# Optimization experiments

Hardware: AMD Instinct MI355X
Metric: run time of the kernel (lower is better)

The kernel has to match this reference:

```python
import jax, jax.numpy as jnp
import numpy as np

N_NODES = 50000
EPS = 1e-16


def seg_softmax(att, seg, n):
    # att: [E, H], softmax over edges sharing the same destination (seg)
    m = jax.ops.segment_max(att, seg, num_segments=n)
    m = jnp.where(jnp.isfinite(m), m, 0.0)
    e = jnp.exp(att - m[seg])
    s = jax.ops.segment_sum(e, seg, num_segments=n)
    return e / (s[seg] + EPS)


def gat_layer(x, W, b, a_l, a_r, row, col, n, nhead, out_feats, alpha, act):
    h = (x @ W).reshape(-1, nhead, out_feats)           # [N, H, F]
    h = jnp.nan_to_num(h)
    h_l = jnp.sum(a_l * h, axis=-1)                     # [N, H]
    h_r = jnp.sum(a_r * h, axis=-1)                     # [N, H]
    e = h_l[row] + h_r[col]                             # [E, H]
    e = jax.nn.leaky_relu(e, negative_slope=alpha)
    att = seg_softmax(e, row, n)                        # softmax per destination node
    # sparse multi-head aggregation: out[i] = sum_{e: row[e]=i} att[e] * h[col[e]]
    msg = att[:, :, None] * h[col]                      # [E, H, F]
    out = jax.ops.segment_sum(msg, row, num_segments=n) # [N, H, F]
    out = out.reshape(n, nhead * out_feats) + b
    if act:
        out = jax.nn.relu(out)
    return out


def setup_inputs() -> dict:
    key = jax.random.key(0)
    ks = jax.random.split(key, 10)
    N, E = N_NODES, 800000
    x = jax.random.normal(ks[0], (N, 256), dtype=jnp.float32)
    row = jax.random.randint(ks[1], (E,), 0, N)
    col = jax.random.randint(ks[2], (E,), 0, N)
    g = 1.414  # xavier-like scale handled via normal * small std
    W1 = jax.random.normal(ks[3], (256, 128), dtype=jnp.float32) * (g / np.sqrt(256 + 128))
    b1 = jnp.zeros((128,), dtype=jnp.float32)
    al1 = jax.random.normal(ks[4], (1, 4, 32), dtype=jnp.float32) * 0.1
    ar1 = jax.random.normal(ks[5], (1, 4, 32), dtype=jnp.float32) * 0.1
    W2 = jax.random.normal(ks[6], (128, 64), dtype=jnp.float32) * (g / np.sqrt(128 + 64))
    b2 = jnp.zeros((64,), dtype=jnp.float32)
    al2 = jax.random.normal(ks[7], (1, 1, 64), dtype=jnp.float32) * 0.1
    ar2 = jax.random.normal(ks[8], (1, 1, 64), dtype=jnp.float32) * 0.1
    return {"x": x, "row": row, "col": col, "W1": W1, "b1": b1, "al1": al1,
            "ar1": ar1, "W2": W2, "b2": b2, "al2": al2, "ar2": ar2}


def reference(x, row, col, W1, b1, al1, ar1, W2, b2, al2, ar2):
    n = N_NODES
    h = gat_layer(x, W1, b1, al1, ar1, row, col, n, nhead=4, out_feats=32, alpha=0.2, act=True)
    out = gat_layer(h, W2, b2, al2, ar2, row, col, n, nhead=1, out_feats=64, alpha=0.2, act=False)
    return out
```

## Files before the change

kernel.cpp:

```cpp
#include <hip/hip_runtime.h>
#include <hip/hip_bf16.h>
#include <hip/hip_fp16.h>
#include <math.h>

#define ALPHA 0.2f
#define LOG2E 1.44269504088896f
#define CAP 8192

typedef _Float16 half8 __attribute__((ext_vector_type(8)));
typedef float f32x4 __attribute__((ext_vector_type(4)));

__global__ __launch_bounds__(256) void setup_kernel(
    int* __restrict__ gcursor,
    const float* __restrict__ W1, _Float16* __restrict__ W1t,
    const float* __restrict__ W2, _Float16* __restrict__ W2t) {
    const int blk = blockIdx.x, tid = threadIdx.x;
    if (blk == 0) {
        gcursor[tid] = 0;
    } else if (blk <= 128) {
        int i = (blk - 1) * 256 + tid;
        int k = i >> 7, c = i & 127;
        W1t[c * 256 + k] = (_Float16)W1[i];
    } else {
        int j = (blk - 129) * 256 + tid;
        int k = j >> 6, c = j & 63;
        W2t[c * 128 + k] = (_Float16)W2[j];
    }
}


__device__ __forceinline__ void part_body(char* smem, int blk,
                                          const int* __restrict__ row,
                                          const int* __restrict__ col,
                                          int* __restrict__ gcursor,
                                          unsigned* __restrict__ tmp, int E) {
    int* h = (int*)smem;
    int* rsv = h + 256;
    const int tid = threadIdx.x;
    const int base = blk * 4096;
    h[tid] = 0;
    __syncthreads();
#pragma unroll
    for (int k = 0; k < 16; ++k) {
        int i = base + k * 256 + tid;
        if (i < E) atomicAdd(&h[row[i] >> 8], 1);
    }
    __syncthreads();
    if (h[tid]) rsv[tid] = atomicAdd(&gcursor[tid], h[tid]);
    __syncthreads();
    h[tid] = 0;
    __syncthreads();
#pragma unroll
    for (int k = 0; k < 16; ++k) {
        int i = base + k * 256 + tid;
        if (i < E) {
            int r = row[i];
            int b = r >> 8;
            int loc = atomicAdd(&h[b], 1);
            tmp[(size_t)b * CAP + rsv[b] + loc] = ((unsigned)r << 16) | (unsigned)col[i];
        }
    }
}

__device__ __forceinline__ void bucket_body(char* smem, int k,
                                            const unsigned* __restrict__ tmp,
                                            const int* __restrict__ gcursor,
                                            unsigned* __restrict__ startcnt,
                                            unsigned short* __restrict__ csr_col, int N) {
    int* h = (int*)smem;
    int* rs = h + 256;
    int* wtot = rs + 256;
    const int tid = threadIdx.x;
    const int lane = tid & 63, wid = tid >> 6;
    const int base = k * CAP;
    const int count = gcursor[k];
    h[tid] = 0;
    __syncthreads();
    for (int p = tid; p < count; p += 256) atomicAdd(&h[(tmp[base + p] >> 16) & 255], 1);
    __syncthreads();
    int v = h[tid];
    int sc = v;
#pragma unroll
    for (int d = 1; d < 64; d <<= 1) {
        int u = __shfl_up(sc, d);
        if (lane >= d) sc += u;
    }
    if (lane == 63) wtot[wid] = sc;
    __syncthreads();
    int add = 0;
    for (int w = 0; w < wid; ++w) add += wtot[w];
    rs[tid] = sc - v + add + base;
    __syncthreads();
    int gr = k * 256 + tid;
    if (gr < N) startcnt[gr] = ((unsigned)rs[tid] << 11) | (unsigned)v;
    h[tid] = 0;
    __syncthreads();
    for (int p = tid; p < count; p += 256) {
        unsigned t = tmp[base + p];
        int rl = (t >> 16) & 255;
        int loc = atomicAdd(&h[rl], 1);
        csr_col[rs[rl] + loc] = (unsigned short)(t & 0xFFFF);
    }
}

__device__ __forceinline__ void gemm1_body(char* smem, int tile,
                                           const float* __restrict__ x,
                                           const _Float16* __restrict__ Wt,
                                           const float* __restrict__ al,
                                           const float* __restrict__ ar,
                                           _Float16* __restrict__ h,
                                           float* __restrict__ hl,
                                           float* __restrict__ hr, int N) {
    _Float16* xs = (_Float16*)smem;
    const int tid = threadIdx.x;
    const int lane = tid & 63, wc = tid >> 6;
    const int row0 = tile * 32;
    const int col0 = wc * 32;

#pragma unroll
    for (int it = 0; it < 8; ++it) {
        int i = it * 256 + tid;
        int r = i >> 6, c4 = i & 63;
        int gr = row0 + r;
        float4 v = {0.f, 0.f, 0.f, 0.f};
        if (gr < N) v = *(const float4*)(x + (size_t)gr * 256 + c4 * 4);
        union { _Float16 p[4]; uint2 u; } pk;
        pk.p[0] = (_Float16)v.x; pk.p[1] = (_Float16)v.y;
        pk.p[2] = (_Float16)v.z; pk.p[3] = (_Float16)v.w;
        int byte = r * 512 + c4 * 8;
        byte ^= (r & 7) << 4;
        *reinterpret_cast<uint2*>(smem + byte) = pk.u;
    }

    const _Float16* wbase = Wt + (size_t)(col0 + (lane & 15)) * 256 + (lane >> 4) * 8;

    __syncthreads();

    f32x4 acc[2][2] = {};
    half8 bf0[2], bf1[2], af0[2], af1[2];

    auto loadB = [&](int s, half8* dst) {
        dst[0] = *(const half8*)(wbase + s * 32);
        dst[1] = *(const half8*)(wbase + 16 * 256 + s * 32);
    };
    auto loadA = [&](int s, half8* dst) {
#pragma unroll
        for (int m = 0; m < 2; ++m) {
            int r = m * 16 + (lane & 15);
            int byte = r * 512 + s * 64 + (lane >> 4) * 16;
            byte ^= (r & 7) << 4;
            dst[m] = *reinterpret_cast<const half8*>(smem + byte);
        }
    };
    auto domfma = [&](half8* a, half8* bvec) {
#pragma unroll
        for (int m = 0; m < 2; ++m)
#pragma unroll
            for (int n = 0; n < 2; ++n)
                acc[m][n] = __builtin_amdgcn_mfma_f32_16x16x32_f16(
                    a[m], bvec[n], acc[m][n], 0, 0, 0);
    };

    loadB(0, bf0); loadA(0, af0);
#pragma unroll
    for (int s = 0; s < 8; s += 2) {
        if (s + 1 < 8) { loadB(s + 1, bf1); loadA(s + 1, af1); }
        domfma(af0, bf0);
        if (s + 2 < 8) { loadB(s + 2, bf0); loadA(s + 2, af0); }
        if (s + 1 < 8) domfma(af1, bf1);
    }

#pragma unroll
    for (int m = 0; m < 2; ++m) {
        int grow_base = row0 + m * 16 + (lane >> 4) * 4;
#pragma unroll
        for (int n = 0; n < 2; ++n) {
            int gcol = col0 + n * 16 + (lane & 15);
#pragma unroll
            for (int reg = 0; reg < 4; ++reg) {
                int grow = grow_base + reg;
                if (grow < N) h[(size_t)grow * 128 + gcol] = (_Float16)acc[m][n][reg];
            }
        }
    }

    const float al0 = al[col0 + (lane & 15)],      ar0 = ar[col0 + (lane & 15)];
    const float al1 = al[col0 + 16 + (lane & 15)], ar1 = ar[col0 + 16 + (lane & 15)];
#pragma unroll
    for (int m = 0; m < 2; ++m) {
#pragma unroll
        for (int reg = 0; reg < 4; ++reg) {
            float l = al0 * acc[m][0][reg] + al1 * acc[m][1][reg];
            float r = ar0 * acc[m][0][reg] + ar1 * acc[m][1][reg];
#pragma unroll
            for (int msk = 1; msk < 16; msk <<= 1) {
                l += __shfl_xor(l, msk);
                r += __shfl_xor(r, msk);
            }
            int grow = row0 + m * 16 + (lane >> 4) * 4 + reg;
            if ((lane & 15) == 0 && grow < N) {
                hl[grow * 4 + wc] = l * LOG2E;
                hr[grow * 4 + wc] = r * LOG2E;
            }
        }
    }
}

__global__ __launch_bounds__(256) void ka_kernel(
    const int* __restrict__ row, const int* __restrict__ col,
    int* __restrict__ gcursor, unsigned* __restrict__ tmp, int E, int eblocks,
    const float* __restrict__ x, const _Float16* __restrict__ W1t,
    const float* __restrict__ al, const float* __restrict__ ar,
    _Float16* __restrict__ h, float* __restrict__ hl, float* __restrict__ hr,
    int N, int tile0)
{
    __shared__ __align__(16) char smem[16384];
    if (blockIdx.x < (unsigned)eblocks)
        part_body(smem, blockIdx.x, row, col, gcursor, tmp, E);
    else
        gemm1_body(smem, tile0 + blockIdx.x - eblocks, x, W1t, al, ar, h, hl, hr, N);
}

__global__ __launch_bounds__(256) void kb_kernel(
    const unsigned* __restrict__ tmp, const int* __restrict__ gcursor,
    unsigned* __restrict__ startcnt, unsigned short* __restrict__ csr_col,
    int nbuck,
    const float* __restrict__ x, const _Float16* __restrict__ W1t,
    const float* __restrict__ al, const float* __restrict__ ar,
    _Float16* __restrict__ h, float* __restrict__ hl, float* __restrict__ hr,
    int N, int tile0)
{
    __shared__ __align__(16) char smem[16384];
    if (blockIdx.x < (unsigned)nbuck)
        bucket_body(smem, blockIdx.x, tmp, gcursor, startcnt, csr_col, N);
    else
        gemm1_body(smem, tile0 + blockIdx.x - nbuck, x, W1t, al, ar, h, hl, hr, N);
}

__global__ __launch_bounds__(256) void gemm2_mfma(
    const _Float16* __restrict__ xin, const _Float16* __restrict__ Wt,
    const float* __restrict__ al, const float* __restrict__ ar,
    _Float16* __restrict__ h, float* __restrict__ hl, float* __restrict__ hr, int N)
{
    __shared__ _Float16 xs[32 * 128];
    __shared__ float plds[32][4], prds[32][4];
    const int tid = threadIdx.x;
    const int lane = tid & 63, wc = tid >> 6;
    const int row0 = blockIdx.x * 32;
    const int col0 = wc * 16;

#pragma unroll
    for (int it = 0; it < 2; ++it) {
        int i = it * 256 + tid;
        int r = i >> 4, c16 = i & 15;
        int gr = row0 + r;
        uint4 v = {0, 0, 0, 0};
        if (gr < N) v = *(const uint4*)(xin + (size_t)gr * 128 + c16 * 8);
        int byte = r * 256 + c16 * 16;
        byte ^= (r & 7) << 4;
        *reinterpret_cast<uint4*>(reinterpret_cast<char*>(xs) + byte) = v;
    }

    const _Float16* wbase = Wt + (size_t)(col0 + (lane & 15)) * 128 + (lane >> 4) * 8;

    __syncthreads();

    f32x4 acc[2] = {};
    half8 bf0, bf1, af0[2], af1[2];

    auto loadA = [&](int s, half8* dst) {
#pragma unroll
        for (int m = 0; m < 2; ++m) {
            int r = m * 16 + (lane & 15);
            int byte = r * 256 + s * 64 + (lane >> 4) * 16;
            byte ^= (r & 7) << 4;
            dst[m] = *reinterpret_cast<const half8*>(
                reinterpret_cast<const char*>(xs) + byte);
        }
    };

    bf0 = *(const half8*)(wbase); loadA(0, af0);
#pragma unroll
    for (int s = 0; s < 4; s += 2) {
        if (s + 1 < 4) { bf1 = *(const half8*)(wbase + (s + 1) * 32); loadA(s + 1, af1); }
#pragma unroll
        for (int m = 0; m < 2; ++m)
            acc[m] = __builtin_amdgcn_mfma_f32_16x16x32_f16(af0[m], bf0, acc[m], 0, 0, 0);
        if (s + 2 < 4) { bf0 = *(const half8*)(wbase + (s + 2) * 32); loadA(s + 2, af0); }
        if (s + 1 < 4)
#pragma unroll
            for (int m = 0; m < 2; ++m)
                acc[m] = __builtin_amdgcn_mfma_f32_16x16x32_f16(af1[m], bf1, acc[m], 0, 0, 0);
    }

#pragma unroll
    for (int m = 0; m < 2; ++m) {
        int grow_base = row0 + m * 16 + (lane >> 4) * 4;
        int gcol = col0 + (lane & 15);
#pragma unroll
        for (int reg = 0; reg < 4; ++reg) {
            int grow = grow_base + reg;
            if (grow < N) h[(size_t)grow * 64 + gcol] = (_Float16)acc[m][reg];
        }
    }

    const float alv = al[col0 + (lane & 15)], arv = ar[col0 + (lane & 15)];
#pragma unroll
    for (int m = 0; m < 2; ++m) {
#pragma unroll
        for (int reg = 0; reg < 4; ++reg) {
            float l = alv * acc[m][reg];
            float r = arv * acc[m][reg];
#pragma unroll
            for (int msk = 1; msk < 16; msk <<= 1) {
                l += __shfl_xor(l, msk);
                r += __shfl_xor(r, msk);
            }
            int ri = m * 16 + (lane >> 4) * 4 + reg;
            if ((lane & 15) == 0) { plds[ri][wc] = l; prds[ri][wc] = r; }
        }
    }
    __syncthreads();
    if (tid < 32) {
        int grow = row0 + tid;
        if (grow < N) {
            float l = plds[tid][0] + plds[tid][1] + plds[tid][2] + plds[tid][3];
            float r = prds[tid][0] + prds[tid][1] + prds[tid][2] + prds[tid][3];
            hl[grow] = l * LOG2E;
            hr[grow] = r * LOG2E;
        }
    }
}

__global__ __launch_bounds__(256) void agg1_kernel(
    const unsigned* __restrict__ startcnt, const unsigned short* __restrict__ csr_col,
    const float* __restrict__ hls, const float* __restrict__ hrs,
    const _Float16* __restrict__ h, const float* __restrict__ b,
    _Float16* __restrict__ out, int N)
{
    const int i = blockIdx.x * 4 + (threadIdx.x >> 6);
    if (i >= N) return;
    const int lane = threadIdx.x & 63;
    const int q = lane >> 4;
    const int fl = lane & 15;
    const int head = fl >> 2;
    const unsigned pk = startcnt[i];
    const int s = (int)(pk >> 11), e = s + (int)(pk & 2047);
    const float hlv = hls[i * 4 + head];

    float acc[8] = {};
    float den = 0.f;

    int p0 = s + q;
    bool v0 = p0 < e;
    int cc0 = v0 ? (int)csr_col[p0] : 0;
    float hr0 = hrs[cc0 * 4 + head];
    uint4 g0 = *(const uint4*)(h + (size_t)cc0 * 128 + 8 * fl);

#pragma unroll 2
    for (int pb = s; pb < e; pb += 4) {
        int p1 = pb + 4 + q;
        bool v1 = p1 < e;
        int cc1 = v1 ? (int)csr_col[p1] : 0;
        float hr1v = hrs[cc1 * 4 + head];
        uint4 g1 = *(const uint4*)(h + (size_t)cc1 * 128 + 8 * fl);

        float sc = hlv + hr0;
        sc = sc > 0.f ? sc : ALPHA * sc;
        float w = exp2f(sc);
        w = v0 ? w : 0.f;
        den += w;
        union { uint4 u; _Float16 q8[8]; } hv; hv.u = g0;
#pragma unroll
        for (int k = 0; k < 8; ++k) acc[k] = fmaf(w, (float)hv.q8[k], acc[k]);

        v0 = v1; cc0 = cc1; hr0 = hr1v; g0 = g1;
    }

    den += __shfl_xor(den, 16); den += __shfl_xor(den, 32);
#pragma unroll
    for (int k = 0; k < 8; ++k) {
        acc[k] += __shfl_xor(acc[k], 16);
        acc[k] += __shfl_xor(acc[k], 32);
    }

    if (lane < 16) {
        float r = 1.f / (den + 1e-16f);
        const float* bp = b + 8 * fl;
        union { uint4 u; _Float16 q8[8]; } ov;
#pragma unroll
        for (int k = 0; k < 8; ++k) {
            float o = acc[k] * r + bp[k];
            o = o > 0.f ? o : 0.f;
            ov.q8[k] = (_Float16)o;
        }
        *reinterpret_cast<uint4*>(out + (size_t)i * 128 + 8 * fl) = ov.u;
    }
}

__global__ __launch_bounds__(256) void agg2_kernel(
    const unsigned* __restrict__ startcnt, const unsigned short* __restrict__ csr_col,
    const float* __restrict__ hls, const float* __restrict__ hrs,
    const _Float16* __restrict__ h, const float* __restrict__ b,
    float* __restrict__ out, int N)
{
    const int i = blockIdx.x * 4 + (threadIdx.x >> 6);
    if (i >= N) return;
    const int lane = threadIdx.x & 63;
    const int q = lane >> 4;
    const int fl = lane & 15;
    const unsigned pk = startcnt[i];
    const int s = (int)(pk >> 11), e = s + (int)(pk & 2047);
    const float hlv = hls[i];

    float acc[4] = {};
    float den = 0.f;

    int p0 = s + q;
    bool v0 = p0 < e;
    int cc0 = v0 ? (int)csr_col[p0] : 0;
    float hr0 = hrs[cc0];
    uint2 g0 = *(const uint2*)(h + (size_t)cc0 * 64 + 4 * fl);

#pragma unroll 2
    for (int pb = s; pb < e; pb += 4) {
        int p1 = pb + 4 + q;
        bool v1 = p1 < e;
        int cc1 = v1 ? (int)csr_col[p1] : 0;
        float hr1v = hrs[cc1];
        uint2 g1 = *(const uint2*)(h + (size_t)cc1 * 64 + 4 * fl);

        float sc = hlv + hr0;
        sc = sc > 0.f ? sc : ALPHA * sc;
        float w = exp2f(sc);
        w = v0 ? w : 0.f;
        den += w;
        union { uint2 u; _Float16 q4[4]; } hv; hv.u = g0;
#pragma unroll
        for (int k = 0; k < 4; ++k) acc[k] = fmaf(w, (float)hv.q4[k], acc[k]);

        v0 = v1; cc0 = cc1; hr0 = hr1v; g0 = g1;
    }

    den += __shfl_xor(den, 16); den += __shfl_xor(den, 32);
#pragma unroll
    for (int k = 0; k < 4; ++k) {
        acc[k] += __shfl_xor(acc[k], 16);
        acc[k] += __shfl_xor(acc[k], 32);
    }

    if (lane < 16) {
        float r = 1.f / (den + 1e-16f);
        float4 bv = *(const float4*)(b + 4 * fl);
        float4 ov;
        ov.x = acc[0] * r + bv.x;
        ov.y = acc[1] * r + bv.y;
        ov.z = acc[2] * r + bv.z;
        ov.w = acc[3] * r + bv.w;
        *reinterpret_cast<float4*>(out + (size_t)i * 64 + 4 * fl) = ov;
    }
}

extern "C" void kernel_launch(void* const* d_in, const int* in_sizes, int n_in,
                              void* d_out, int out_size, void* d_ws, size_t ws_size,
                              hipStream_t stream)
{
    const float* x   = (const float*)d_in[0];
    const int*   row = (const int*)d_in[1];
    const int*   col = (const int*)d_in[2];
    const float* W1  = (const float*)d_in[3];
    const float* b1  = (const float*)d_in[4];
    const float* al1 = (const float*)d_in[5];
    const float* ar1 = (const float*)d_in[6];
    const float* W2  = (const float*)d_in[7];
    const float* b2  = (const float*)d_in[8];
    const float* al2 = (const float*)d_in[9];
    const float* ar2 = (const float*)d_in[10];
    const int N = in_sizes[0] / 256;
    const int E = in_sizes[1];
    const int nbuck = (N + 255) >> 8;
    float* out = (float*)d_out;

    size_t off_b = 0;
    auto alloc = [&](size_t bytes) -> void* {
        void* p = (char*)d_ws + off_b;
        off_b += (bytes + 255) & ~(size_t)255;
        return p;
    };
    int*            gcursor  = (int*)alloc((size_t)256 * 4);
    unsigned*       startcnt = (unsigned*)alloc((size_t)N * 4);
    unsigned*       tmp      = (unsigned*)alloc((size_t)nbuck * CAP * 4);
    unsigned short* csr_col  = (unsigned short*)alloc((size_t)nbuck * CAP * 2 + 32);
    _Float16*       W1t      = (_Float16*)alloc((size_t)128 * 256 * 2);
    _Float16*       W2t      = (_Float16*)alloc((size_t)64 * 128 * 2);
    _Float16*       h1       = (_Float16*)alloc((size_t)N * 128 * 2);
    float*          hl1      = (float*)alloc((size_t)N * 4 * 4);
    float*          hr1      = (float*)alloc((size_t)N * 4 * 4);
    _Float16*       out1h    = (_Float16*)alloc((size_t)N * 128 * 2);
    _Float16*       h2       = (_Float16*)alloc((size_t)N * 64 * 2);
    float*          hl2      = (float*)alloc((size_t)N * 4);
    float*          hr2      = (float*)alloc((size_t)N * 4);
    (void)ws_size; (void)n_in; (void)out_size;

    const int eblocks = (E + 4095) / 4096;
    const int tiles = (N + 31) / 32;
    const int tilesA = (tiles + 1) / 2;
    const int tilesB = tiles - tilesA;

    setup_kernel<<<161, 256, 0, stream>>>(gcursor, W1, W1t, W2, W2t);
    ka_kernel<<<eblocks + tilesA, 256, 0, stream>>>(row, col, gcursor, tmp, E, eblocks,
                                                    x, W1t, al1, ar1, h1, hl1, hr1, N, 0);
    kb_kernel<<<nbuck + tilesB, 256, 0, stream>>>(tmp, gcursor, startcnt, csr_col, nbuck,
                                                  x, W1t, al1, ar1, h1, hl1, hr1, N, tilesA);

    agg1_kernel<<<(N + 3) / 4, 256, 0, stream>>>(startcnt, csr_col, hl1, hr1, h1, b1, out1h, N);

    gemm2_mfma<<<(N + 31) / 32, 256, 0, stream>>>(out1h, W2t, al2, ar2, h2, hl2, hr2, N);
    agg2_kernel<<<(N + 3) / 4, 256, 0, stream>>>(startcnt, csr_col, hl2, hr2, h2, b2, out, N);
}
```

Before: 121.5 us.

## Fuse layer-1 aggregation with layer-2 GEMM via shared-memory row tile

Merges the first-layer attention aggregation kernel into the second-layer MFMA GEMM. Each block aggregates 32 nodes, 8 per wave, writing the biased, ReLU'd fp16 rows straight into a swizzled shared-memory tile that the GEMM then consumes. This drops the out1h global round trip and one kernel launch. The cost is fewer blocks (one per 32 nodes instead of one per 4) and a serial loop of 8 nodes per wave, which cuts the memory-level parallelism available to the latency-bound gather.

```diff
diff --git a/kernel.cpp b/kernel.cpp
--- a/kernel.cpp
+++ b/kernel.cpp
@@ -111,7 +111,6 @@
                                            _Float16* __restrict__ h,
                                            float* __restrict__ hl,
                                            float* __restrict__ hr, int N) {
-    _Float16* xs = (_Float16*)smem;
     const int tid = threadIdx.x;
     const int lane = tid & 63, wc = tid >> 6;
     const int row0 = tile * 32;
@@ -237,35 +236,96 @@
         gemm1_body(smem, tile0 + blockIdx.x - nbuck, x, W1t, al, ar, h, hl, hr, N);
 }
 
-__global__ __launch_bounds__(256) void gemm2_mfma(
-    const _Float16* __restrict__ xin, const _Float16* __restrict__ Wt,
+__global__ __launch_bounds__(256) void agg1g2_kernel(
+    const unsigned* __restrict__ startcnt, const unsigned short* __restrict__ csr_col,
+    const float* __restrict__ hls, const float* __restrict__ hrs,
+    const _Float16* __restrict__ h, const float* __restrict__ b,
+    const _Float16* __restrict__ W2t,
     const float* __restrict__ al, const float* __restrict__ ar,
-    _Float16* __restrict__ h, float* __restrict__ hl, float* __restrict__ hr, int N)
+    _Float16* __restrict__ h2, float* __restrict__ hl2, float* __restrict__ hr2, int N)
 {
-    __shared__ _Float16 xs[32 * 128];
+    __shared__ __align__(16) char rows[32 * 256];
     __shared__ float plds[32][4], prds[32][4];
     const int tid = threadIdx.x;
-    const int lane = tid & 63, wc = tid >> 6;
-    const int row0 = blockIdx.x * 32;
+    const int lane = tid & 63, wid = tid >> 6;
+    const int node0 = blockIdx.x * 32;
+    const int q = lane >> 4;
+    const int fl = lane & 15;
+    const int head = fl >> 2;
+
+    float bp[8];
+#pragma unroll
+    for (int k = 0; k < 8; ++k) bp[k] = b[8 * fl + k];
+
+    for (int j = 0; j < 8; ++j) {
+        const int i = node0 + wid * 8 + j;
+        const int r = wid * 8 + j;
+        float acc[8] = {};
+        float den = 0.f;
+        bool live = i < N;
+        if (live) {
+            const unsigned pk = startcnt[i];
+            const int s = (int)(pk >> 11), e = s + (int)(pk & 2047);
+            const float hlv = hls[i * 4 + head];
+
+            int p0 = s + q;
+            bool v0 = p0 < e;
+            int cc0 = v0 ? (int)csr_col[p0] : 0;
+            float hr0 = hrs[cc0 * 4 + head];
+            uint4 g0 = *(const uint4*)(h + (size_t)cc0 * 128 + 8 * fl);
+
+#pragma unroll 2
+            for (int pb = s; pb < e; pb += 4) {
+                int p1 = pb + 4 + q;
+                bool v1 = p1 < e;
+                int cc1 = v1 ? (int)csr_col[p1] : 0;
+                float hr1v = hrs[cc1 * 4 + head];
+                uint4 g1 = *(const uint4*)(h + (size_t)cc1 * 128 + 8 * fl);
+
+                float sc = hlv + hr0;
+                sc = sc > 0.f ? sc : ALPHA * sc;
+                float w = exp2f(sc);
+                w = v0 ? w : 0.f;
+                den += w;
+                union { uint4 u; _Float16 q8[8]; } hv; hv.u = g0;
+#pragma unroll
+                for (int k = 0; k < 8; ++k) acc[k] = fmaf(w, (float)hv.q8[k], acc[k]);
+
+                v0 = v1; cc0 = cc1; hr0 = hr1v; g0 = g1;
+            }
+
+            den += __shfl_xor(den, 16); den += __shfl_xor(den, 32);
+#pragma unroll
+            for (int k = 0; k < 8; ++k) {
+                acc[k] += __shfl_xor(acc[k], 16);
+                acc[k] += __shfl_xor(acc[k], 32);
+            }
+        }
+        if (lane < 16) {
+            union { uint4 u; _Float16 q8[8]; } ov;
+            if (live) {
+                float rcp = 1.f / (den + 1e-16f);
+#pragma unroll
+                for (int k = 0; k < 8; ++k) {
+                    float o = acc[k] * rcp + bp[k];
+                    o = o > 0.f ? o : 0.f;
+                    ov.q8[k] = (_Float16)o;
+                }
+            } else {
+                ov.u = make_uint4(0, 0, 0, 0);
+            }
+            int byte = r * 256 + fl * 16;
+            byte ^= (r & 7) << 4;
+            *reinterpret_cast<uint4*>(rows + byte) = ov.u;
+        }
+    }
+    __syncthreads();
+
+    const int wc = wid;
     const int col0 = wc * 16;
-
-#pragma unroll
-    for (int it = 0; it < 2; ++it) {
-        int i = it * 256 + tid;
-        int r = i >> 4, c16 = i & 15;
-        int gr = row0 + r;
-        uint4 v = {0, 0, 0, 0};
-        if (gr < N) v = *(const uint4*)(xin + (size_t)gr * 128 + c16 * 8);
-        int byte = r * 256 + c16 * 16;
-        byte ^= (r & 7) << 4;
-        *reinterpret_cast<uint4*>(reinterpret_cast<char*>(xs) + byte) = v;
-    }
-
-    const _Float16* wbase = Wt + (size_t)(col0 + (lane & 15)) * 128 + (lane >> 4) * 8;
-
-    __syncthreads();
-
-    f32x4 acc[2] = {};
+    const _Float16* wbase = W2t + (size_t)(col0 + (lane & 15)) * 128 + (lane >> 4) * 8;
+
+    f32x4 acc2[2] = {};
     half8 bf0, bf1, af0[2], af1[2];
 
     auto loadA = [&](int s, half8* dst) {
@@ -274,8 +334,7 @@
             int r = m * 16 + (lane & 15);
             int byte = r * 256 + s * 64 + (lane >> 4) * 16;
             byte ^= (r & 7) << 4;
-            dst[m] = *reinterpret_cast<const half8*>(
-                reinterpret_cast<const char*>(xs) + byte);
+            dst[m] = *reinterpret_cast<const half8*>(rows + byte);
         }
     };
 
@@ -285,22 +344,22 @@
         if (s + 1 < 4) { bf1 = *(const half8*)(wbase + (s + 1) * 32); loadA(s + 1, af1); }
 #pragma unroll
         for (int m = 0; m < 2; ++m)
-            acc[m] = __builtin_amdgcn_mfma_f32_16x16x32_f16(af0[m], bf0, acc[m], 0, 0, 0);
+            acc2[m] = __builtin_amdgcn_mfma_f32_16x16x32_f16(af0[m], bf0, acc2[m], 0, 0, 0);
         if (s + 2 < 4) { bf0 = *(const half8*)(wbase + (s + 2) * 32); loadA(s + 2, af0); }
         if (s + 1 < 4)
 #pragma unroll
             for (int m = 0; m < 2; ++m)
-                acc[m] = __builtin_amdgcn_mfma_f32_16x16x32_f16(af1[m], bf1, acc[m], 0, 0, 0);
+                acc2[m] = __builtin_amdgcn_mfma_f32_16x16x32_f16(af1[m], bf1, acc2[m], 0, 0, 0);
     }
 
 #pragma unroll
     for (int m = 0; m < 2; ++m) {
-        int grow_base = row0 + m * 16 + (lane >> 4) * 4;
+        int grow_base = node0 + m * 16 + (lane >> 4) * 4;
         int gcol = col0 + (lane & 15);
 #pragma unroll
         for (int reg = 0; reg < 4; ++reg) {
             int grow = grow_base + reg;
-            if (grow < N) h[(size_t)grow * 64 + gcol] = (_Float16)acc[m][reg];
+            if (grow < N) h2[(size_t)grow * 64 + gcol] = (_Float16)acc2[m][reg];
         }
     }
 
@@ -309,8 +368,8 @@
     for (int m = 0; m < 2; ++m) {
 #pragma unroll
         for (int reg = 0; reg < 4; ++reg) {
-            float l = alv * acc[m][reg];
-            float r = arv * acc[m][reg];
+            float l = alv * acc2[m][reg];
+            float r = arv * acc2[m][reg];
 #pragma unroll
             for (int msk = 1; msk < 16; msk <<= 1) {
                 l += __shfl_xor(l, msk);
@@ -322,79 +381,13 @@
     }
     __syncthreads();
     if (tid < 32) {
-        int grow = row0 + tid;
+        int grow = node0 + tid;
         if (grow < N) {
             float l = plds[tid][0] + plds[tid][1] + plds[tid][2] + plds[tid][3];
             float r = prds[tid][0] + prds[tid][1] + prds[tid][2] + prds[tid][3];
-            hl[grow] = l * LOG2E;
-            hr[grow] = r * LOG2E;
-        }
-    }
-}
-
-__global__ __launch_bounds__(256) void agg1_kernel(
-    const unsigned* __restrict__ startcnt, const unsigned short* __restrict__ csr_col,
-    const float* __restrict__ hls, const float* __restrict__ hrs,
-    const _Float16* __restrict__ h, const float* __restrict__ b,
-    _Float16* __restrict__ out, int N)
-{
-    const int i = blockIdx.x * 4 + (threadIdx.x >> 6);
-    if (i >= N) return;
-    const int lane = threadIdx.x & 63;
-    const int q = lane >> 4;
-    const int fl = lane & 15;
-    const int head = fl >> 2;
-    const unsigned pk = startcnt[i];
-    const int s = (int)(pk >> 11), e = s + (int)(pk & 2047);
-    const float hlv = hls[i * 4 + head];
-
-    float acc[8] = {};
-    float den = 0.f;
-
-    int p0 = s + q;
-    bool v0 = p0 < e;
-    int cc0 = v0 ? (int)csr_col[p0] : 0;
-    float hr0 = hrs[cc0 * 4 + head];
-    uint4 g0 = *(const uint4*)(h + (size_t)cc0 * 128 + 8 * fl);
-
-#pragma unroll 2
-    for (int pb = s; pb < e; pb += 4) {
-        int p1 = pb + 4 + q;
-        bool v1 = p1 < e;
-        int cc1 = v1 ? (int)csr_col[p1] : 0;
-        float hr1v = hrs[cc1 * 4 + head];
-        uint4 g1 = *(const uint4*)(h + (size_t)cc1 * 128 + 8 * fl);
-
-        float sc = hlv + hr0;
-        sc = sc > 0.f ? sc : ALPHA * sc;
-        float w = exp2f(sc);
-        w = v0 ? w : 0.f;
-        den += w;
-        union { uint4 u; _Float16 q8[8]; } hv; hv.u = g0;
-#pragma unroll
-        for (int k = 0; k < 8; ++k) acc[k] = fmaf(w, (float)hv.q8[k], acc[k]);
-
-        v0 = v1; cc0 = cc1; hr0 = hr1v; g0 = g1;
-    }
-
-    den += __shfl_xor(den, 16); den += __shfl_xor(den, 32);
-#pragma unroll
-    for (int k = 0; k < 8; ++k) {
-        acc[k] += __shfl_xor(acc[k], 16);
-        acc[k] += __shfl_xor(acc[k], 32);
-    }
-
-    if (lane < 16) {
-        float r = 1.f / (den + 1e-16f);
-        const float* bp = b + 8 * fl;
-        union { uint4 u; _Float16 q8[8]; } ov;
-#pragma unroll
-        for (int k = 0; k < 8; ++k) {
-            float o = acc[k] * r + bp[k];
-            o = o > 0.f ? o : 0.f;
-            ov.q8[k] = (_Float16)o;
-        }
-        *reinterpret_cast<uint4*>(out + (size_t)i * 128 + 8 * fl) = ov.u;
+            hl2[grow] = l * LOG2E;
+            hr2[grow] = r * LOG2E;
+        }
     }
 }
 
@@ -496,7 +489,6 @@
     _Float16*       h1       = (_Float16*)alloc((size_t)N * 128 * 2);
     float*          hl1      = (float*)alloc((size_t)N * 4 * 4);
     float*          hr1      = (float*)alloc((size_t)N * 4 * 4);
-    _Float16*       out1h    = (_Float16*)alloc((size_t)N * 128 * 2);
     _Float16*       h2       = (_Float16*)alloc((size_t)N * 64 * 2);
     float*          hl2      = (float*)alloc((size_t)N * 4);
     float*          hr2      = (float*)alloc((size_t)N * 4);
@@ -513,8 +505,8 @@
     kb_kernel<<<nbuck + tilesB, 256, 0, stream>>>(tmp, gcursor, startcnt, csr_col, nbuck,
                                                   x, W1t, al1, ar1, h1, hl1, hr1, N, tilesA);
 
-    agg1_kernel<<<(N + 3) / 4, 256, 0, stream>>>(startcnt, csr_col, hl1, hr1, h1, b1, out1h, N);
-
-    gemm2_mfma<<<(N + 31) / 32, 256, 0, stream>>>(out1h, W2t, al2, ar2, h2, hl2, hr2, N);
+    agg1g2_kernel<<<(N + 31) / 32, 256, 0, stream>>>(startcnt, csr_col, hl1, hr1, h1, b1,
+                                                     W2t, al2, ar2, h2, hl2, hr2, N);
+
     agg2_kernel<<<(N + 3) / 4, 256, 0, stream>>>(startcnt, csr_col, hl2, hr2, h2, b2, out, N);
 }
```

Result: faster. 116.0 us (-4.5%).
